# Performance work log

Measured on AMD Instinct MI355X. Metric: run time of the kernel, lower is better.

## Reference

```python
import jax, jax.numpy as jnp
import numpy as np

N, IN_DIM, HIDDEN, L = 20000, 128, 256, 6
ALPHA = 0.1
EPS = 1e-5

def setup_inputs() -> dict:
    key = jax.random.key(0)
    ks = jax.random.split(key, 8)
    x = jax.random.normal(ks[0], (N, IN_DIM), dtype=jnp.float32)
    E = 320000
    src = jax.random.randint(ks[1], (E,), 0, N)
    dst = jax.random.randint(ks[2], (E,), 0, N)
    edge_index = jnp.stack([src, dst], axis=0)
    s = 1.0 / np.sqrt(IN_DIM)
    W_in = jax.random.normal(ks[3], (IN_DIM, HIDDEN), dtype=jnp.float32) * s
    b_in = jnp.zeros((HIDDEN,), dtype=jnp.float32)
    g_in = jnp.ones((HIDDEN,), dtype=jnp.float32)
    beta_in = jnp.zeros((HIDDEN,), dtype=jnp.float32)
    sc = 1.0 / np.sqrt(HIDDEN)
    Wc = jax.random.normal(ks[4], (L, HIDDEN, HIDDEN), dtype=jnp.float32) * sc
    bc = jnp.zeros((L, HIDDEN), dtype=jnp.float32)
    gc = jnp.ones((L, HIDDEN), dtype=jnp.float32)
    betac = jnp.zeros((L, HIDDEN), dtype=jnp.float32)
    return {"x": x, "edge_index": edge_index, "W_in": W_in, "b_in": b_in,
            "g_in": g_in, "beta_in": beta_in, "Wc": Wc, "bc": bc,
            "gc": gc, "betac": betac}

def _layer_norm(h, g, b):
    mu = jnp.mean(h, axis=-1, keepdims=True)
    var = jnp.mean((h - mu) ** 2, axis=-1, keepdims=True)
    return (h - mu) * jax.lax.rsqrt(var + EPS) * g + b

def _gcn_norm(edge_index, n):
    # add self loops (weight 1), symmetric normalization
    loop = jnp.arange(n, dtype=edge_index.dtype)
    row = jnp.concatenate([edge_index[0], loop])
    col = jnp.concatenate([edge_index[1], loop])
    w = jnp.ones((row.shape[0],), dtype=jnp.float32)
    deg = jax.ops.segment_sum(w, col, num_segments=n)
    dinv = jnp.where(deg > 0, jax.lax.rsqrt(deg), 0.0)
    norm = dinv[row] * w * dinv[col]
    return row, col, norm

def reference(x, edge_index, W_in, b_in, g_in, beta_in, Wc, bc, gc, betac):
    n = x.shape[0]
    row, col, norm = _gcn_norm(edge_index, n)
    # input block: Linear -> GELU -> LayerNorm (dropout = eval identity)
    h = _layer_norm(jax.nn.gelu(x @ W_in + b_in), g_in, beta_in)
    h0 = h
    xcur = h
    for l in range(L):
        z = xcur @ Wc[l]                              # [N, H]
        agg = jax.ops.segment_sum(z[row] * norm[:, None], col, num_segments=n)
        out = agg + bc[l]
        out = _layer_norm(jax.nn.gelu(out), gc[l], betac[l])
        hblend = (1.0 - ALPHA) * out + ALPHA * h0
        xcur = xcur + hblend
    return xcur
```

## Files before the change

kernel.cpp:

```cpp
#include <hip/hip_runtime.h>
#include <hip/hip_bf16.h>
#include <math.h>

#define HID 256
typedef __attribute__((ext_vector_type(8))) short s16x8;
typedef __attribute__((ext_vector_type(4))) float f32x4;

__device__ __forceinline__ ushort f2bf(float f){
    uint u = __float_as_uint(f);
    u += 0x7FFF + ((u>>16)&1);
    return (ushort)(u>>16);
}
__device__ __forceinline__ float bf2f(ushort b){
    return __uint_as_float(((uint)b)<<16);
}
__device__ __forceinline__ float4 bf4_to_f4(ushort4 u){
    return make_float4(bf2f(u.x), bf2f(u.y), bf2f(u.z), bf2f(u.w));
}

__device__ __forceinline__ float gelu_tanh(float x){
    float u = 0.7978845608028654f*(x + 0.044715f*x*x*x);
    float t = 1.0f - 2.0f/(1.0f + __expf(2.0f*u));
    return 0.5f*x*(1.0f+t);
}

__global__ void k_count(const int* __restrict__ dst, int* __restrict__ cnt, int E){
    int e = blockIdx.x*blockDim.x + threadIdx.x;
    if(e<E) atomicAdd(&cnt[dst[e]], 1);
}

__global__ __launch_bounds__(256) void k_scan1(const int* __restrict__ cnt,
    int* __restrict__ tsum, int* __restrict__ bsum, int N){
    __shared__ int sm[256];
    int t = threadIdx.x, b = blockIdx.x;
    int base = b*1024 + t*4;
    int c0=0,c1=0,c2=0,c3=0;
    if(base+3 < N){
        int4 c = *reinterpret_cast<const int4*>(&cnt[base]);
        c0=c.x; c1=c.y; c2=c.z; c3=c.w;
    }else{
        if(base  <N) c0=cnt[base];
        if(base+1<N) c1=cnt[base+1];
        if(base+2<N) c2=cnt[base+2];
        if(base+3<N) c3=cnt[base+3];
    }
    int s = c0+c1+c2+c3;
    sm[t]=s; __syncthreads();
    for(int off=1; off<256; off<<=1){
        int v = sm[t];
        int a = (t>=off)? sm[t-off] : 0;
        __syncthreads();
        sm[t] = v+a;
        __syncthreads();
    }
    tsum[b*256+t] = sm[t]-s;
    if(t==255) bsum[b] = sm[255];
}

__global__ __launch_bounds__(256) void k_scan3(const int* __restrict__ cnt,
    const int* __restrict__ tsum, const int* __restrict__ bsum,
    int* __restrict__ indptr, int* __restrict__ cursor, float* __restrict__ dinv,
    int N, int B){
    __shared__ int sboff, stot;
    int t = threadIdx.x, b = blockIdx.x;
    if(t==0){
        int run=0, tot=0;
        for(int i=0;i<B;i++){ int v=bsum[i]; if(i<b) run+=v; tot+=v; }
        sboff=run; stot=tot;
        if(b==0) indptr[N]=tot;
    }
    __syncthreads();
    int base = b*1024 + t*4;
    int run = sboff + tsum[b*256+t];
    #pragma unroll
    for(int i=0;i<4;i++){
        int idx = base+i;
        if(idx<N){
            int c = cnt[idx];
            indptr[idx]=run; cursor[idx]=run;
            dinv[idx] = rsqrtf((float)(c+1));
            run += c;
        }
    }
}

__global__ void k_fill(const int* __restrict__ src, const int* __restrict__ dst,
    int* __restrict__ cursor, int* __restrict__ csr, int E){
    int e = blockIdx.x*blockDim.x + threadIdx.x;
    if(e<E){
        int pos = atomicAdd(&cursor[dst[e]], 1);
        csr[pos] = src[e];
    }
}

__global__ void k_cvt_w(const float* __restrict__ Win, const float* __restrict__ Wc,
    ushort* __restrict__ wbin, ushort* __restrict__ wbc){
    int i = blockIdx.x*blockDim.x + threadIdx.x;
    if(i < 32768){
        int k = i >> 8, n = i & 255;
        int kb = k>>5, hi=(k>>3)&3, ii=k&7;
        wbin[((kb*256+n)*4+hi)*8 + ii] = f2bf(Win[i]);
    }else if(i < 32768 + 6*65536){
        int j = i - 32768;
        int l = j >> 16;
        int k = (j>>8)&255, n = j&255;
        int kb = k>>5, hi=(k>>3)&3, ii=k&7;
        wbc[l*65536 + ((kb*256+n)*4+hi)*8 + ii] = f2bf(Wc[j]);
    }
}

__global__ __launch_bounds__(256) void k_agg(const ushort* __restrict__ xb,
    const int* __restrict__ indptr, const int* __restrict__ csr,
    const float* __restrict__ dinv, ushort* __restrict__ yb, int N)
{
    int wave = threadIdx.x>>6, lane = threadIdx.x&63;
    int n = blockIdx.x*4 + wave;
    if(n>=N) return;
    const ushort4* X4 = reinterpret_cast<const ushort4*>(xb);
    float dn = dinv[n];
    float4 sv = bf4_to_f4(X4[(size_t)n*64+lane]);
    float4 acc = make_float4(dn*sv.x, dn*sv.y, dn*sv.z, dn*sv.w);
    int e0 = indptr[n], e1 = indptr[n+1];
    int e = e0;
    for(; e+8<=e1; e+=8){
        int idx[8];
        #pragma unroll
        for(int q=0;q<8;q++) idx[q]=csr[e+q];
        float4 v[8]; float dv[8];
        #pragma unroll
        for(int q=0;q<8;q++){ v[q]=bf4_to_f4(X4[(size_t)idx[q]*64+lane]); dv[q]=dinv[idx[q]]; }
        #pragma unroll
        for(int q=0;q<8;q++){
            acc.x = fmaf(dv[q],v[q].x,acc.x);
            acc.y = fmaf(dv[q],v[q].y,acc.y);
            acc.z = fmaf(dv[q],v[q].z,acc.z);
            acc.w = fmaf(dv[q],v[q].w,acc.w);
        }
    }
    if(e+4<=e1){
        int i0=csr[e], i1=csr[e+1], i2=csr[e+2], i3=csr[e+3];
        float4 v0 = bf4_to_f4(X4[(size_t)i0*64+lane]); float d0=dinv[i0];
        float4 v1 = bf4_to_f4(X4[(size_t)i1*64+lane]); float d1=dinv[i1];
        float4 v2 = bf4_to_f4(X4[(size_t)i2*64+lane]); float d2=dinv[i2];
        float4 v3 = bf4_to_f4(X4[(size_t)i3*64+lane]); float d3=dinv[i3];
        acc.x += d0*v0.x + d1*v1.x + d2*v2.x + d3*v3.x;
        acc.y += d0*v0.y + d1*v1.y + d2*v2.y + d3*v3.y;
        acc.z += d0*v0.z + d1*v1.z + d2*v2.z + d3*v3.z;
        acc.w += d0*v0.w + d1*v1.w + d2*v2.w + d3*v3.w;
        e += 4;
    }
    for(; e<e1; e++){
        int s = csr[e];
        float4 v = bf4_to_f4(X4[(size_t)s*64+lane]); float d=dinv[s];
        acc.x = fmaf(d,v.x,acc.x); acc.y = fmaf(d,v.y,acc.y);
        acc.z = fmaf(d,v.z,acc.z); acc.w = fmaf(d,v.w,acc.w);
    }
    ushort4 o; o.x=f2bf(dn*acc.x); o.y=f2bf(dn*acc.y); o.z=f2bf(dn*acc.z); o.w=f2bf(dn*acc.w);
    reinterpret_cast<ushort4*>(yb)[(size_t)n*64+lane] = o;
}

template<int MODE>
__device__ __forceinline__ void epilogue16(f32x4 (&acc)[4],
    const float* __restrict__ bp, const float* __restrict__ gp, const float* __restrict__ bep,
    ushort* __restrict__ h0b, ushort* __restrict__ xb, float* __restrict__ fout,
    int row0, int wc, int lr, int hi, int N,
    float (*sm1)[4], float (*sm2)[4])
{
    float bcv[4], gcv[4], bev[4];
    #pragma unroll
    for(int nf=0;nf<4;nf++){
        int col = wc*64 + nf*16 + lr;
        bcv[nf]=bp[col]; gcv[nf]=gp[col]; bev[nf]=bep[col];
    }
    #pragma unroll
    for(int r=0;r<4;r++){
        float ls1=0.f, ls2=0.f;
        #pragma unroll
        for(int nf=0;nf<4;nf++){
            float t = gelu_tanh(acc[nf][r] + bcv[nf]);
            acc[nf][r] = t;
            ls1 += t; ls2 += t*t;
        }
        #pragma unroll
        for(int off=1; off<16; off<<=1){
            ls1 += __shfl_xor(ls1, off, 64);
            ls2 += __shfl_xor(ls2, off, 64);
        }
        if(lr==0){
            int row = hi*4 + r;
            sm1[row][wc]=ls1; sm2[row][wc]=ls2;
        }
    }
    __syncthreads();
    #pragma unroll
    for(int r=0;r<4;r++){
        int row = hi*4 + r;
        int grow = row0 + row;
        if(grow >= N) continue;
        float S1 = sm1[row][0]+sm1[row][1]+sm1[row][2]+sm1[row][3];
        float S2 = sm2[row][0]+sm2[row][1]+sm2[row][2]+sm2[row][3];
        float mu = S1*(1.0f/256.0f);
        float var = fmaxf(S2*(1.0f/256.0f) - mu*mu, 0.0f);
        float rs = rsqrtf(var + 1e-5f);
        #pragma unroll
        for(int nf=0;nf<4;nf++){
            int col = wc*64 + nf*16 + lr;
            size_t idx = (size_t)grow*HID + col;
            float o = (acc[nf][r]-mu)*rs*gcv[nf] + bev[nf];
            if(MODE==0){
                ushort ob = f2bf(o);
                h0b[idx] = ob;
                xb[idx] = ob;
            }else{
                float xc = bf2f(xb[idx]) + 0.9f*o + 0.1f*bf2f(h0b[idx]);
                if(MODE==1) xb[idx] = f2bf(xc);
                else        fout[idx] = xc;
            }
        }
    }
}

__global__ __launch_bounds__(256) void k_gemm_in(const float* __restrict__ X,
    const ushort* __restrict__ Wb,
    const float* __restrict__ bp, const float* __restrict__ gp, const float* __restrict__ bep,
    ushort* __restrict__ h0b, ushort* __restrict__ xb, int N)
{
    const int lane = threadIdx.x & 63;
    const int wc = threadIdx.x >> 6;
    const int lr = lane & 15;
    const int hi = lane >> 4;
    const int row0 = blockIdx.x*16;
    __shared__ float sm1[16][4];
    __shared__ float sm2[16][4];

    f32x4 acc[4];
    #pragma unroll
    for(int n=0;n<4;n++){ acc[n].x=0.f; acc[n].y=0.f; acc[n].z=0.f; acc[n].w=0.f; }

    int r0 = row0 + lr; if(r0 >= N) r0 = N-1;
    const float* xp0 = X + (size_t)r0*128 + hi*8;
    const ushort* bpp = Wb + (wc*64 + lr)*32 + hi*8;

    #pragma unroll
    for(int kb=0; kb<4; kb++){
        float4 p0a = *reinterpret_cast<const float4*>(xp0 + kb*32);
        float4 p0b = *reinterpret_cast<const float4*>(xp0 + kb*32 + 4);
        s16x8 a0;
        a0[0]=(short)f2bf(p0a.x); a0[1]=(short)f2bf(p0a.y); a0[2]=(short)f2bf(p0a.z); a0[3]=(short)f2bf(p0a.w);
        a0[4]=(short)f2bf(p0b.x); a0[5]=(short)f2bf(p0b.y); a0[6]=(short)f2bf(p0b.z); a0[7]=(short)f2bf(p0b.w);
        #pragma unroll
        for(int nf=0;nf<4;nf++){
            s16x8 b = *reinterpret_cast<const s16x8*>(bpp + kb*8192 + nf*512);
            acc[nf] = __builtin_amdgcn_mfma_f32_16x16x32_bf16(a0, b, acc[nf], 0,0,0);
        }
    }
    epilogue16<0>(acc, bp, gp, bep, h0b, xb, nullptr, row0, wc, lr, hi, N, sm1, sm2);
}

template<int MODE>
__global__ __launch_bounds__(256) void k_gemm_fused(const ushort* __restrict__ A,
    const ushort* __restrict__ Wb,
    const float* __restrict__ bp, const float* __restrict__ gp, const float* __restrict__ bep,
    ushort* __restrict__ h0b, ushort* __restrict__ xb, float* __restrict__ fout, int N)
{
    const int lane = threadIdx.x & 63;
    const int wc = threadIdx.x >> 6;
    const int lr = lane & 15;
    const int hi = lane >> 4;
    const int row0 = blockIdx.x*16;
    __shared__ float sm1[16][4];
    __shared__ float sm2[16][4];

    f32x4 acc[4];
    #pragma unroll
    for(int n=0;n<4;n++){ acc[n].x=0.f; acc[n].y=0.f; acc[n].z=0.f; acc[n].w=0.f; }

    int r0 = row0 + lr; if(r0 >= N) r0 = N-1;
    const ushort* ap0 = A + (size_t)r0*256 + hi*8;
    const ushort* bpp = Wb + (wc*64 + lr)*32 + hi*8;

    s16x8 a0[2], bb[2][4];
    a0[0] = *reinterpret_cast<const s16x8*>(ap0);
    #pragma unroll
    for(int nf=0;nf<4;nf++) bb[0][nf] = *reinterpret_cast<const s16x8*>(bpp + nf*512);

    #pragma unroll
    for(int kb=0; kb<8; kb++){
        const int cur = kb&1, nxt = cur^1;
        if(kb < 7){
            a0[nxt] = *reinterpret_cast<const s16x8*>(ap0 + (kb+1)*32);
            #pragma unroll
            for(int nf=0;nf<4;nf++)
                bb[nxt][nf] = *reinterpret_cast<const s16x8*>(bpp + (kb+1)*8192 + nf*512);
        }
        #pragma unroll
        for(int nf=0;nf<4;nf++)
            acc[nf] = __builtin_amdgcn_mfma_f32_16x16x32_bf16(a0[cur], bb[cur][nf], acc[nf], 0,0,0);
    }
    epilogue16<MODE>(acc, bp, gp, bep, h0b, xb, fout, row0, wc, lr, hi, N, sm1, sm2);
}

extern "C" void kernel_launch(void* const* d_in, const int* in_sizes, int n_in,
                              void* d_out, int out_size, void* d_ws, size_t ws_size,
                              hipStream_t stream){
    const float* x     = (const float*)d_in[0];
    const int*   ei    = (const int*)d_in[1];
    const float* W_in  = (const float*)d_in[2];
    const float* b_in  = (const float*)d_in[3];
    const float* g_in  = (const float*)d_in[4];
    const float* be_in = (const float*)d_in[5];
    const float* Wc    = (const float*)d_in[6];
    const float* bc    = (const float*)d_in[7];
    const float* gc    = (const float*)d_in[8];
    const float* bec   = (const float*)d_in[9];
    const int N = in_sizes[0]/128;
    const int E = in_sizes[1]/2;
    const int* src = ei;
    const int* dst = ei + E;
    float* fout = (float*)d_out;
    const int B = (N+1023)/1024;

    char* w = (char*)d_ws;
    ushort* xb   = (ushort*)w; w += (size_t)N*HID*2;
    ushort* yb   = (ushort*)w; w += (size_t)N*HID*2;
    ushort* h0b  = (ushort*)w; w += (size_t)N*HID*2;
    ushort* wbin = (ushort*)w; w += (size_t)128*256*2;
    ushort* wbc  = (ushort*)w; w += (size_t)6*65536*2;
    float* dinv  = (float*)w;  w += (size_t)N*4;
    int* cnt     = (int*)w;    w += (size_t)N*4;
    int* cursor  = (int*)w;    w += (size_t)N*4;
    int* csr     = (int*)w;    w += (size_t)E*4;
    int* indptr  = (int*)w;    w += (size_t)(N+1)*4;
    int* tsum    = (int*)w;    w += (size_t)B*256*4;
    int* bsum    = (int*)w;    w += (size_t)B*4;

    (void)hipMemsetAsync(cnt, 0, (size_t)N*4, stream);
    k_count<<<(E+255)/256,256,0,stream>>>(dst,cnt,E);
    k_scan1<<<B,256,0,stream>>>(cnt, tsum, bsum, N);
    k_scan3<<<B,256,0,stream>>>(cnt, tsum, bsum, indptr, cursor, dinv, N, B);
    k_fill<<<(E+255)/256,256,0,stream>>>(src,dst,cursor,csr,E);
    k_cvt_w<<<(32768+6*65536+255)/256,256,0,stream>>>(W_in, Wc, wbin, wbc);

    const int GB = (N+15)/16;
    k_gemm_in<<<GB,256,0,stream>>>(x, wbin, b_in, g_in, be_in, h0b, xb, N);
    for(int l=0;l<6;l++){
        k_agg<<<(N+3)/4,256,0,stream>>>(xb, indptr, csr, dinv, yb, N);
        if(l<5)
            k_gemm_fused<1><<<GB,256,0,stream>>>(yb, wbc+(size_t)l*65536,
                bc+(size_t)l*HID, gc+(size_t)l*HID, bec+(size_t)l*HID,
                h0b, xb, nullptr, N);
        else
            k_gemm_fused<2><<<GB,256,0,stream>>>(yb, wbc+(size_t)l*65536,
                bc+(size_t)l*HID, gc+(size_t)l*HID, bec+(size_t)l*HID,
                h0b, xb, fout, N);
    }
}
```

Baseline: 336.1 us.

## Fuse neighbor aggregation with GEMM and LayerNorm epilogue into one per-layer kernel

Each layer's sparse aggregation, GEMM, GELU/LayerNorm and residual blend now run in a single 1024-thread kernel. Aggregated rows go to swizzled LDS and are fed straight to MFMA, with K split across two wave groups and reduced in LDS. The x buffer is ping-ponged so gathers read the old features while the new ones are written. This removes the intermediate yb round trip and one launch per layer. The cost is heavier blocks with larger LDS use, which may limit occupancy, and the weight slices are reloaded by every block.

```diff
diff --git a/kernel.cpp b/kernel.cpp
--- a/kernel.cpp
+++ b/kernel.cpp
@@ -61,12 +61,12 @@
     const int* __restrict__ tsum, const int* __restrict__ bsum,
     int* __restrict__ indptr, int* __restrict__ cursor, float* __restrict__ dinv,
     int N, int B){
-    __shared__ int sboff, stot;
+    __shared__ int sboff;
     int t = threadIdx.x, b = blockIdx.x;
     if(t==0){
         int run=0, tot=0;
         for(int i=0;i<B;i++){ int v=bsum[i]; if(i<b) run+=v; tot+=v; }
-        sboff=run; stot=tot;
+        sboff=run;
         if(b==0) indptr[N]=tot;
     }
     __syncthreads();
@@ -109,60 +109,9 @@
     }
 }
 
-__global__ __launch_bounds__(256) void k_agg(const ushort* __restrict__ xb,
-    const int* __restrict__ indptr, const int* __restrict__ csr,
-    const float* __restrict__ dinv, ushort* __restrict__ yb, int N)
-{
-    int wave = threadIdx.x>>6, lane = threadIdx.x&63;
-    int n = blockIdx.x*4 + wave;
-    if(n>=N) return;
-    const ushort4* X4 = reinterpret_cast<const ushort4*>(xb);
-    float dn = dinv[n];
-    float4 sv = bf4_to_f4(X4[(size_t)n*64+lane]);
-    float4 acc = make_float4(dn*sv.x, dn*sv.y, dn*sv.z, dn*sv.w);
-    int e0 = indptr[n], e1 = indptr[n+1];
-    int e = e0;
-    for(; e+8<=e1; e+=8){
-        int idx[8];
-        #pragma unroll
-        for(int q=0;q<8;q++) idx[q]=csr[e+q];
-        float4 v[8]; float dv[8];
-        #pragma unroll
-        for(int q=0;q<8;q++){ v[q]=bf4_to_f4(X4[(size_t)idx[q]*64+lane]); dv[q]=dinv[idx[q]]; }
-        #pragma unroll
-        for(int q=0;q<8;q++){
-            acc.x = fmaf(dv[q],v[q].x,acc.x);
-            acc.y = fmaf(dv[q],v[q].y,acc.y);
-            acc.z = fmaf(dv[q],v[q].z,acc.z);
-            acc.w = fmaf(dv[q],v[q].w,acc.w);
-        }
-    }
-    if(e+4<=e1){
-        int i0=csr[e], i1=csr[e+1], i2=csr[e+2], i3=csr[e+3];
-        float4 v0 = bf4_to_f4(X4[(size_t)i0*64+lane]); float d0=dinv[i0];
-        float4 v1 = bf4_to_f4(X4[(size_t)i1*64+lane]); float d1=dinv[i1];
-        float4 v2 = bf4_to_f4(X4[(size_t)i2*64+lane]); float d2=dinv[i2];
-        float4 v3 = bf4_to_f4(X4[(size_t)i3*64+lane]); float d3=dinv[i3];
-        acc.x += d0*v0.x + d1*v1.x + d2*v2.x + d3*v3.x;
-        acc.y += d0*v0.y + d1*v1.y + d2*v2.y + d3*v3.y;
-        acc.z += d0*v0.z + d1*v1.z + d2*v2.z + d3*v3.z;
-        acc.w += d0*v0.w + d1*v1.w + d2*v2.w + d3*v3.w;
-        e += 4;
-    }
-    for(; e<e1; e++){
-        int s = csr[e];
-        float4 v = bf4_to_f4(X4[(size_t)s*64+lane]); float d=dinv[s];
-        acc.x = fmaf(d,v.x,acc.x); acc.y = fmaf(d,v.y,acc.y);
-        acc.z = fmaf(d,v.z,acc.z); acc.w = fmaf(d,v.w,acc.w);
-    }
-    ushort4 o; o.x=f2bf(dn*acc.x); o.y=f2bf(dn*acc.y); o.z=f2bf(dn*acc.z); o.w=f2bf(dn*acc.w);
-    reinterpret_cast<ushort4*>(yb)[(size_t)n*64+lane] = o;
-}
-
-template<int MODE>
-__device__ __forceinline__ void epilogue16(f32x4 (&acc)[4],
+__device__ __forceinline__ void epilogue_in(f32x4 (&acc)[4],
     const float* __restrict__ bp, const float* __restrict__ gp, const float* __restrict__ bep,
-    ushort* __restrict__ h0b, ushort* __restrict__ xb, float* __restrict__ fout,
+    ushort* __restrict__ h0b, ushort* __restrict__ xb,
     int row0, int wc, int lr, int hi, int N,
     float (*sm1)[4], float (*sm2)[4])
 {
@@ -207,15 +156,9 @@
             int col = wc*64 + nf*16 + lr;
             size_t idx = (size_t)grow*HID + col;
             float o = (acc[nf][r]-mu)*rs*gcv[nf] + bev[nf];
-            if(MODE==0){
-                ushort ob = f2bf(o);
-                h0b[idx] = ob;
-                xb[idx] = ob;
-            }else{
-                float xc = bf2f(xb[idx]) + 0.9f*o + 0.1f*bf2f(h0b[idx]);
-                if(MODE==1) xb[idx] = f2bf(xc);
-                else        fout[idx] = xc;
-            }
+            ushort ob = f2bf(o);
+            h0b[idx] = ob;
+            xb[idx] = ob;
         }
     }
 }
@@ -254,50 +197,129 @@
             acc[nf] = __builtin_amdgcn_mfma_f32_16x16x32_bf16(a0, b, acc[nf], 0,0,0);
         }
     }
-    epilogue16<0>(acc, bp, gp, bep, h0b, xb, nullptr, row0, wc, lr, hi, N, sm1, sm2);
+    epilogue_in(acc, bp, gp, bep, h0b, xb, row0, wc, lr, hi, N, sm1, sm2);
 }
 
 template<int MODE>
-__global__ __launch_bounds__(256) void k_gemm_fused(const ushort* __restrict__ A,
+__global__ __launch_bounds__(1024, 8) void k_layer(const ushort* __restrict__ xbA,
     const ushort* __restrict__ Wb,
+    const int* __restrict__ indptr, const int* __restrict__ csr,
+    const float* __restrict__ dinv,
     const float* __restrict__ bp, const float* __restrict__ gp, const float* __restrict__ bep,
-    ushort* __restrict__ h0b, ushort* __restrict__ xb, float* __restrict__ fout, int N)
+    const ushort* __restrict__ h0b, ushort* __restrict__ xbB, float* __restrict__ fout, int N)
 {
-    const int lane = threadIdx.x & 63;
-    const int wc = threadIdx.x >> 6;
-    const int lr = lane & 15;
-    const int hi = lane >> 4;
+    __shared__ ushort als[16*256];
+    __shared__ float yls[2*16*256];
+    const int tid = threadIdx.x;
+    const int w = tid >> 6;
+    const int lane = tid & 63;
     const int row0 = blockIdx.x*16;
-    __shared__ float sm1[16][4];
-    __shared__ float sm2[16][4];
-
-    f32x4 acc[4];
-    #pragma unroll
-    for(int n=0;n<4;n++){ acc[n].x=0.f; acc[n].y=0.f; acc[n].z=0.f; acc[n].w=0.f; }
-
-    int r0 = row0 + lr; if(r0 >= N) r0 = N-1;
-    const ushort* ap0 = A + (size_t)r0*256 + hi*8;
-    const ushort* bpp = Wb + (wc*64 + lr)*32 + hi*8;
-
-    s16x8 a0[2], bb[2][4];
-    a0[0] = *reinterpret_cast<const s16x8*>(ap0);
-    #pragma unroll
-    for(int nf=0;nf<4;nf++) bb[0][nf] = *reinterpret_cast<const s16x8*>(bpp + nf*512);
-
-    #pragma unroll
-    for(int kb=0; kb<8; kb++){
-        const int cur = kb&1, nxt = cur^1;
-        if(kb < 7){
-            a0[nxt] = *reinterpret_cast<const s16x8*>(ap0 + (kb+1)*32);
-            #pragma unroll
-            for(int nf=0;nf<4;nf++)
-                bb[nxt][nf] = *reinterpret_cast<const s16x8*>(bpp + (kb+1)*8192 + nf*512);
-        }
-        #pragma unroll
-        for(int nf=0;nf<4;nf++)
-            acc[nf] = __builtin_amdgcn_mfma_f32_16x16x32_bf16(a0[cur], bb[cur][nf], acc[nf], 0,0,0);
-    }
-    epilogue16<MODE>(acc, bp, gp, bep, h0b, xb, fout, row0, wc, lr, hi, N, sm1, sm2);
+    char* ab = (char*)als;
+
+    {
+        int n = row0 + w; if(n >= N) n = N-1;
+        float dn = dinv[n];
+        const ushort4* X4 = reinterpret_cast<const ushort4*>(xbA);
+        float4 sv = bf4_to_f4(X4[(size_t)n*64 + lane]);
+        float4 acc = make_float4(dn*sv.x, dn*sv.y, dn*sv.z, dn*sv.w);
+        int e0 = indptr[n], e1 = indptr[n+1];
+        int e = e0;
+        for(; e+8<=e1; e+=8){
+            int idx[8];
+            #pragma unroll
+            for(int q=0;q<8;q++) idx[q]=csr[e+q];
+            float4 v[8]; float dv[8];
+            #pragma unroll
+            for(int q=0;q<8;q++){ v[q]=bf4_to_f4(X4[(size_t)idx[q]*64+lane]); dv[q]=dinv[idx[q]]; }
+            #pragma unroll
+            for(int q=0;q<8;q++){
+                acc.x = fmaf(dv[q],v[q].x,acc.x);
+                acc.y = fmaf(dv[q],v[q].y,acc.y);
+                acc.z = fmaf(dv[q],v[q].z,acc.z);
+                acc.w = fmaf(dv[q],v[q].w,acc.w);
+            }
+        }
+        for(; e<e1; e++){
+            int s = csr[e];
+            float4 v = bf4_to_f4(X4[(size_t)s*64+lane]); float d=dinv[s];
+            acc.x = fmaf(d,v.x,acc.x); acc.y = fmaf(d,v.y,acc.y);
+            acc.z = fmaf(d,v.z,acc.z); acc.w = fmaf(d,v.w,acc.w);
+        }
+        ushort4 o; o.x=f2bf(dn*acc.x); o.y=f2bf(dn*acc.y); o.z=f2bf(dn*acc.z); o.w=f2bf(dn*acc.w);
+        *reinterpret_cast<ushort4*>(ab + w*512 + ((lane*8) ^ ((w&7)<<4))) = o;
+    }
+    __syncthreads();
+
+    {
+        const int kq = w >> 3, wc = w & 7;
+        const int lr = lane & 15, hi = lane >> 4;
+        f32x4 acc2[2];
+        #pragma unroll
+        for(int nf=0;nf<2;nf++){ acc2[nf].x=0.f; acc2[nf].y=0.f; acc2[nf].z=0.f; acc2[nf].w=0.f; }
+        const ushort* bpp = Wb + (wc*32 + lr)*32 + hi*8;
+        const int sws = (lr&7)<<4;
+        #pragma unroll
+        for(int kbl=0; kbl<4; kbl++){
+            int kb = kq*4 + kbl;
+            int cb = kb*64 + hi*16;
+            s16x8 a = *reinterpret_cast<const s16x8*>(ab + lr*512 + (cb ^ sws));
+            s16x8 b0 = *reinterpret_cast<const s16x8*>(bpp + kb*8192);
+            s16x8 b1 = *reinterpret_cast<const s16x8*>(bpp + kb*8192 + 512);
+            acc2[0] = __builtin_amdgcn_mfma_f32_16x16x32_bf16(a, b0, acc2[0], 0,0,0);
+            acc2[1] = __builtin_amdgcn_mfma_f32_16x16x32_bf16(a, b1, acc2[1], 0,0,0);
+        }
+        float* yb_ = yls + kq*4096;
+        #pragma unroll
+        for(int nf=0;nf<2;nf++){
+            #pragma unroll
+            for(int r=0;r<4;r++)
+                yb_[(hi*4+r)*256 + wc*32 + nf*16 + lr] = acc2[nf][r];
+        }
+    }
+    __syncthreads();
+
+    {
+        int grow = row0 + w;
+        if(grow < N){
+            float4 t0 = *reinterpret_cast<const float4*>(&yls[w*256 + lane*4]);
+            float4 t1 = *reinterpret_cast<const float4*>(&yls[4096 + w*256 + lane*4]);
+            float4 bb4 = *reinterpret_cast<const float4*>(&bp[lane*4]);
+            float4 t;
+            t.x = gelu_tanh(t0.x+t1.x+bb4.x);
+            t.y = gelu_tanh(t0.y+t1.y+bb4.y);
+            t.z = gelu_tanh(t0.z+t1.z+bb4.z);
+            t.w = gelu_tanh(t0.w+t1.w+bb4.w);
+            float s1 = t.x+t.y+t.z+t.w;
+            float s2 = t.x*t.x+t.y*t.y+t.z*t.z+t.w*t.w;
+            #pragma unroll
+            for(int off=32; off>0; off>>=1){
+                s1 += __shfl_xor(s1, off, 64);
+                s2 += __shfl_xor(s2, off, 64);
+            }
+            float mu = s1*(1.0f/256.0f);
+            float var = fmaxf(s2*(1.0f/256.0f) - mu*mu, 0.0f);
+            float rs = rsqrtf(var + 1e-5f);
+            float4 gg = *reinterpret_cast<const float4*>(&gp[lane*4]);
+            float4 be4 = *reinterpret_cast<const float4*>(&bep[lane*4]);
+            float4 o;
+            o.x = (t.x-mu)*rs*gg.x + be4.x;
+            o.y = (t.y-mu)*rs*gg.y + be4.y;
+            o.z = (t.z-mu)*rs*gg.z + be4.z;
+            o.w = (t.w-mu)*rs*gg.w + be4.w;
+            float4 h = bf4_to_f4(reinterpret_cast<const ushort4*>(h0b)[(size_t)grow*64+lane]);
+            float4 xc = bf4_to_f4(reinterpret_cast<const ushort4*>(xbA)[(size_t)grow*64+lane]);
+            xc.x += 0.9f*o.x + 0.1f*h.x;
+            xc.y += 0.9f*o.y + 0.1f*h.y;
+            xc.z += 0.9f*o.z + 0.1f*h.z;
+            xc.w += 0.9f*o.w + 0.1f*h.w;
+            if(MODE==1){
+                ushort4 ob; ob.x=f2bf(xc.x); ob.y=f2bf(xc.y); ob.z=f2bf(xc.z); ob.w=f2bf(xc.w);
+                reinterpret_cast<ushort4*>(xbB)[(size_t)grow*64+lane] = ob;
+            }else{
+                reinterpret_cast<float4*>(fout)[(size_t)grow*64+lane] = xc;
+            }
+        }
+    }
 }
 
 extern "C" void kernel_launch(void* const* d_in, const int* in_sizes, int n_in,
@@ -321,8 +343,8 @@
     const int B = (N+1023)/1024;
 
     char* w = (char*)d_ws;
-    ushort* xb   = (ushort*)w; w += (size_t)N*HID*2;
-    ushort* yb   = (ushort*)w; w += (size_t)N*HID*2;
+    ushort* xb0  = (ushort*)w; w += (size_t)N*HID*2;
+    ushort* xb1  = (ushort*)w; w += (size_t)N*HID*2;
     ushort* h0b  = (ushort*)w; w += (size_t)N*HID*2;
     ushort* wbin = (ushort*)w; w += (size_t)128*256*2;
     ushort* wbc  = (ushort*)w; w += (size_t)6*65536*2;
@@ -335,23 +357,26 @@
     int* bsum    = (int*)w;    w += (size_t)B*4;
 
     (void)hipMemsetAsync(cnt, 0, (size_t)N*4, stream);
+    k_cvt_w<<<(32768+6*65536+255)/256,256,0,stream>>>(W_in, Wc, wbin, wbc);
     k_count<<<(E+255)/256,256,0,stream>>>(dst,cnt,E);
     k_scan1<<<B,256,0,stream>>>(cnt, tsum, bsum, N);
     k_scan3<<<B,256,0,stream>>>(cnt, tsum, bsum, indptr, cursor, dinv, N, B);
     k_fill<<<(E+255)/256,256,0,stream>>>(src,dst,cursor,csr,E);
-    k_cvt_w<<<(32768+6*65536+255)/256,256,0,stream>>>(W_in, Wc, wbin, wbc);
 
     const int GB = (N+15)/16;
-    k_gemm_in<<<GB,256,0,stream>>>(x, wbin, b_in, g_in, be_in, h0b, xb, N);
+    k_gemm_in<<<GB,256,0,stream>>>(x, wbin, b_in, g_in, be_in, h0b, xb0, N);
+    ushort* xsA = xb0;
+    ushort* xsB = xb1;
     for(int l=0;l<6;l++){
-        k_agg<<<(N+3)/4,256,0,stream>>>(xb, indptr, csr, dinv, yb, N);
-        if(l<5)
-            k_gemm_fused<1><<<GB,256,0,stream>>>(yb, wbc+(size_t)l*65536,
+        if(l<5){
+            k_layer<1><<<GB,1024,0,stream>>>(xsA, wbc+(size_t)l*65536, indptr, csr, dinv,
                 bc+(size_t)l*HID, gc+(size_t)l*HID, bec+(size_t)l*HID,
-                h0b, xb, nullptr, N);
-        else
-            k_gemm_fused<2><<<GB,256,0,stream>>>(yb, wbc+(size_t)l*65536,
+                h0b, xsB, nullptr, N);
+        }else{
+            k_layer<2><<<GB,1024,0,stream>>>(xsA, wbc+(size_t)l*65536, indptr, csr, dinv,
                 bc+(size_t)l*HID, gc+(size_t)l*HID, bec+(size_t)l*HID,
-                h0b, xb, fout, N);
-    }
-}
+                h0b, nullptr, fout, N);
+        }
+        ushort* t = xsA; xsA = xsB; xsB = t;
+    }
+}
```

Measured after the change: 351.7 us. 4.6% more time.

## Split aggregation wave into two half-waves with 16-byte gathers; merge weight-convert and count kernels

Applied to the files above, without the earlier changes.

The aggregation kernel now has each half of a wave gather a different neighbor row. Each lane loads 8 bf16 values (16 bytes) instead of 4, and the two halves are combined with a cross-lane shuffle at the end. This doubles the neighbor rows in flight per wave and widens each load, at the cost of a shuffle reduction, odd-edge handling, and half the lanes idling on the final store. Separately, the weight conversion and the edge-degree counting are fused into one launch to save a kernel launch.

```diff
diff --git a/kernel.cpp b/kernel.cpp
--- a/kernel.cpp
+++ b/kernel.cpp
@@ -4,6 +4,7 @@
 
 #define HID 256
 typedef __attribute__((ext_vector_type(8))) short s16x8;
+typedef __attribute__((ext_vector_type(8))) ushort u16x8;
 typedef __attribute__((ext_vector_type(4))) float f32x4;
 
 __device__ __forceinline__ ushort f2bf(float f){
@@ -24,9 +25,28 @@
     return 0.5f*x*(1.0f+t);
 }
 
-__global__ void k_count(const int* __restrict__ dst, int* __restrict__ cnt, int E){
-    int e = blockIdx.x*blockDim.x + threadIdx.x;
-    if(e<E) atomicAdd(&cnt[dst[e]], 1);
+#define CVTB 1664
+__global__ void k_cvt_count(const float* __restrict__ Win, const float* __restrict__ Wc,
+    ushort* __restrict__ wbin, ushort* __restrict__ wbc,
+    const int* __restrict__ dst, int* __restrict__ cnt, int E){
+    int b = blockIdx.x;
+    if(b < CVTB){
+        int i = b*256 + threadIdx.x;
+        if(i < 32768){
+            int k = i >> 8, n = i & 255;
+            int kb = k>>5, hi=(k>>3)&3, ii=k&7;
+            wbin[((kb*256+n)*4+hi)*8 + ii] = f2bf(Win[i]);
+        }else{
+            int j = i - 32768;
+            int l = j >> 16;
+            int k = (j>>8)&255, n = j&255;
+            int kb = k>>5, hi=(k>>3)&3, ii=k&7;
+            wbc[l*65536 + ((kb*256+n)*4+hi)*8 + ii] = f2bf(Wc[j]);
+        }
+    }else{
+        int e = (b-CVTB)*256 + threadIdx.x;
+        if(e<E) atomicAdd(&cnt[dst[e]], 1);
+    }
 }
 
 __global__ __launch_bounds__(256) void k_scan1(const int* __restrict__ cnt,
@@ -61,12 +81,12 @@
     const int* __restrict__ tsum, const int* __restrict__ bsum,
     int* __restrict__ indptr, int* __restrict__ cursor, float* __restrict__ dinv,
     int N, int B){
-    __shared__ int sboff, stot;
+    __shared__ int sboff;
     int t = threadIdx.x, b = blockIdx.x;
     if(t==0){
         int run=0, tot=0;
         for(int i=0;i<B;i++){ int v=bsum[i]; if(i<b) run+=v; tot+=v; }
-        sboff=run; stot=tot;
+        sboff=run;
         if(b==0) indptr[N]=tot;
     }
     __syncthreads();
@@ -93,22 +113,6 @@
     }
 }
 
-__global__ void k_cvt_w(const float* __restrict__ Win, const float* __restrict__ Wc,
-    ushort* __restrict__ wbin, ushort* __restrict__ wbc){
-    int i = blockIdx.x*blockDim.x + threadIdx.x;
-    if(i < 32768){
-        int k = i >> 8, n = i & 255;
-        int kb = k>>5, hi=(k>>3)&3, ii=k&7;
-        wbin[((kb*256+n)*4+hi)*8 + ii] = f2bf(Win[i]);
-    }else if(i < 32768 + 6*65536){
-        int j = i - 32768;
-        int l = j >> 16;
-        int k = (j>>8)&255, n = j&255;
-        int kb = k>>5, hi=(k>>3)&3, ii=k&7;
-        wbc[l*65536 + ((kb*256+n)*4+hi)*8 + ii] = f2bf(Wc[j]);
-    }
-}
-
 __global__ __launch_bounds__(256) void k_agg(const ushort* __restrict__ xb,
     const int* __restrict__ indptr, const int* __restrict__ csr,
     const float* __restrict__ dinv, ushort* __restrict__ yb, int N)
@@ -116,47 +120,57 @@
     int wave = threadIdx.x>>6, lane = threadIdx.x&63;
     int n = blockIdx.x*4 + wave;
     if(n>=N) return;
-    const ushort4* X4 = reinterpret_cast<const ushort4*>(xb);
+    const u16x8* X8 = reinterpret_cast<const u16x8*>(xb);
+    const int half = lane >> 5;
+    const int l = lane & 31;
     float dn = dinv[n];
-    float4 sv = bf4_to_f4(X4[(size_t)n*64+lane]);
-    float4 acc = make_float4(dn*sv.x, dn*sv.y, dn*sv.z, dn*sv.w);
+    float acc[8];
+    {
+        u16x8 v = X8[(size_t)n*32 + l];
+        float w0 = (half==0)? dn : 0.f;
+        #pragma unroll
+        for(int j=0;j<8;j++) acc[j] = w0 * bf2f(v[j]);
+    }
     int e0 = indptr[n], e1 = indptr[n+1];
     int e = e0;
     for(; e+8<=e1; e+=8){
-        int idx[8];
-        #pragma unroll
-        for(int q=0;q<8;q++) idx[q]=csr[e+q];
-        float4 v[8]; float dv[8];
-        #pragma unroll
-        for(int q=0;q<8;q++){ v[q]=bf4_to_f4(X4[(size_t)idx[q]*64+lane]); dv[q]=dinv[idx[q]]; }
-        #pragma unroll
-        for(int q=0;q<8;q++){
-            acc.x = fmaf(dv[q],v[q].x,acc.x);
-            acc.y = fmaf(dv[q],v[q].y,acc.y);
-            acc.z = fmaf(dv[q],v[q].z,acc.z);
-            acc.w = fmaf(dv[q],v[q].w,acc.w);
-        }
-    }
-    if(e+4<=e1){
-        int i0=csr[e], i1=csr[e+1], i2=csr[e+2], i3=csr[e+3];
-        float4 v0 = bf4_to_f4(X4[(size_t)i0*64+lane]); float d0=dinv[i0];
-        float4 v1 = bf4_to_f4(X4[(size_t)i1*64+lane]); float d1=dinv[i1];
-        float4 v2 = bf4_to_f4(X4[(size_t)i2*64+lane]); float d2=dinv[i2];
-        float4 v3 = bf4_to_f4(X4[(size_t)i3*64+lane]); float d3=dinv[i3];
-        acc.x += d0*v0.x + d1*v1.x + d2*v2.x + d3*v3.x;
-        acc.y += d0*v0.y + d1*v1.y + d2*v2.y + d3*v3.y;
-        acc.z += d0*v0.z + d1*v1.z + d2*v2.z + d3*v3.z;
-        acc.w += d0*v0.w + d1*v1.w + d2*v2.w + d3*v3.w;
-        e += 4;
-    }
-    for(; e<e1; e++){
-        int s = csr[e];
-        float4 v = bf4_to_f4(X4[(size_t)s*64+lane]); float d=dinv[s];
-        acc.x = fmaf(d,v.x,acc.x); acc.y = fmaf(d,v.y,acc.y);
-        acc.z = fmaf(d,v.z,acc.z); acc.w = fmaf(d,v.w,acc.w);
-    }
-    ushort4 o; o.x=f2bf(dn*acc.x); o.y=f2bf(dn*acc.y); o.z=f2bf(dn*acc.z); o.w=f2bf(dn*acc.w);
-    reinterpret_cast<ushort4*>(yb)[(size_t)n*64+lane] = o;
+        int is[4];
+        #pragma unroll
+        for(int q=0;q<4;q++) is[q] = csr[e + q*2 + half];
+        u16x8 vs[4];
+        #pragma unroll
+        for(int q=0;q<4;q++) vs[q] = X8[(size_t)is[q]*32 + l];
+        float ds[4];
+        #pragma unroll
+        for(int q=0;q<4;q++) ds[q] = dinv[is[q]];
+        #pragma unroll
+        for(int q=0;q<4;q++){
+            #pragma unroll
+            for(int j=0;j<8;j++) acc[j] = fmaf(ds[q], bf2f(vs[q][j]), acc[j]);
+        }
+    }
+    for(; e+2<=e1; e+=2){
+        int i = csr[e + half];
+        u16x8 v = X8[(size_t)i*32 + l];
+        float d = dinv[i];
+        #pragma unroll
+        for(int j=0;j<8;j++) acc[j] = fmaf(d, bf2f(v[j]), acc[j]);
+    }
+    if(e<e1){
+        int i = csr[e];
+        u16x8 v = X8[(size_t)i*32 + l];
+        float d = (half==0)? dinv[i] : 0.f;
+        #pragma unroll
+        for(int j=0;j<8;j++) acc[j] = fmaf(d, bf2f(v[j]), acc[j]);
+    }
+    #pragma unroll
+    for(int j=0;j<8;j++) acc[j] += __shfl_xor(acc[j], 32, 64);
+    if(half==0){
+        u16x8 o;
+        #pragma unroll
+        for(int j=0;j<8;j++) o[j] = f2bf(dn*acc[j]);
+        reinterpret_cast<u16x8*>(yb)[(size_t)n*32 + l] = o;
+    }
 }
 
 template<int MODE>
@@ -335,11 +349,10 @@
     int* bsum    = (int*)w;    w += (size_t)B*4;
 
     (void)hipMemsetAsync(cnt, 0, (size_t)N*4, stream);
-    k_count<<<(E+255)/256,256,0,stream>>>(dst,cnt,E);
+    k_cvt_count<<<CVTB + (E+255)/256,256,0,stream>>>(W_in, Wc, wbin, wbc, dst, cnt, E);
     k_scan1<<<B,256,0,stream>>>(cnt, tsum, bsum, N);
     k_scan3<<<B,256,0,stream>>>(cnt, tsum, bsum, indptr, cursor, dinv, N, B);
     k_fill<<<(E+255)/256,256,0,stream>>>(src,dst,cursor,csr,E);
-    k_cvt_w<<<(32768+6*65536+255)/256,256,0,stream>>>(W_in, Wc, wbin, wbc);
 
     const int GB = (N+15)/16;
     k_gemm_in<<<GB,256,0,stream>>>(x, wbin, b_in, g_in, be_in, h0b, xb, N);
```

New measurement: 326.7 us. -2.8%, faster.
